# Kernel optimization log

Measured on AMD Instinct MI355X. Metric: run time of the kernel, lower is better.

Reference implementation:

```python
import jax, jax.numpy as jnp
import numpy as np

B, N, T = 1, 1024, 2048   # batch, graph nodes, timesteps
E, K = 16384, 32          # edges, causal kernel taps


def setup_inputs() -> dict:
    key = jax.random.key(0)
    k1, k2, k3, k4 = jax.random.split(key, 4)
    x = jax.random.normal(k1, (B, N, T), dtype=jnp.float32)
    # per-edge causal impulse-response kernels (aggregator(g) output)
    kernel = jax.random.normal(k2, (E, K), dtype=jnp.float32) * 0.1
    src = jax.random.randint(k3, (E,), 0, N)
    dst = jax.random.randint(k4, (E,), 0, N)
    return {"x": x, "kernel": kernel, "src": src, "dst": dst}


def reference(x, kernel, src, dst):
    # Block-sparse causal conv over the edge list:
    #   y_e[b, t] = sum_k kernel[e, k] * x[b, src_e, t - k]   (causal)
    #   out[b, n, t] = x[b, n, t] + sum_{e: dst_e = n} y_e[b, t]
    # (residual applied because g.include_index_diag is False)
    xs = x[:, src, :]                      # [B, E, T] gather upstream signals
    rhs = kernel[:, None, ::-1]            # [E, 1, K] flipped -> true causal conv
    y = jax.lax.conv_general_dilated(
        xs, rhs,
        window_strides=(1,),
        padding=[(K - 1, 0)],              # left-pad: strictly causal
        dimension_numbers=("NCW", "OIW", "NCW"),
        feature_group_count=E,             # one independent kernel per edge
    )                                      # [B, E, T]
    agg = jax.ops.segment_sum(jnp.swapaxes(y, 0, 1), dst, num_segments=N)  # [N, B, T]
    return x + jnp.swapaxes(agg, 0, 1)     # [B, N, T]
```

## Files before the change

kernel.cpp:

```cpp
#include <hip/hip_runtime.h>
#include <hip/hip_bf16.h>

#define TT  2048
#define KK  32
#define NN  1024
#define EE  16384
#define CAP 64
#define RS  2080

typedef short short8  __attribute__((ext_vector_type(8)));
typedef short short4v __attribute__((ext_vector_type(4)));
typedef float f32x4   __attribute__((ext_vector_type(4)));

__device__ short g_xbf[NN * RS];
__device__ short g_kbf[EE * KK];

__device__ __forceinline__ short f2bf(float f) {
    __hip_bfloat16 h = __float2bfloat16(f);
    return __builtin_bit_cast(short, h);
}

__global__ __launch_bounds__(256) void cvt_kernel(const float* __restrict__ x,
                                                  const float* __restrict__ kern,
                                                  int* __restrict__ cnt) {
    const int bid = blockIdx.x, tid = threadIdx.x;
    if (bid < NN) {
        const float4* xr = (const float4*)(x + (size_t)bid * TT);
        const float4 u = xr[2 * tid], v = xr[2 * tid + 1];
        short8 h;
        h[0]=f2bf(u.x); h[1]=f2bf(u.y); h[2]=f2bf(u.z); h[3]=f2bf(u.w);
        h[4]=f2bf(v.x); h[5]=f2bf(v.y); h[6]=f2bf(v.z); h[7]=f2bf(v.w);
        *(short8*)&g_xbf[(size_t)bid * RS + 32 + 8 * tid] = h;
        if (tid < 4) {
            short8 z; z[0]=0;z[1]=0;z[2]=0;z[3]=0;z[4]=0;z[5]=0;z[6]=0;z[7]=0;
            *(short8*)&g_xbf[(size_t)bid * RS + 8 * tid] = z;
        }
    } else if (bid == NN) {
        ((int4*)cnt)[tid] = make_int4(0, 0, 0, 0);
    } else {
        const int i = (bid - NN - 1) * 256 + tid;
        const float4* k4 = (const float4*)kern;
        const float4 u = k4[2 * i], v = k4[2 * i + 1];
        short8 h;
        h[0]=f2bf(u.x); h[1]=f2bf(u.y); h[2]=f2bf(u.z); h[3]=f2bf(u.w);
        h[4]=f2bf(v.x); h[5]=f2bf(v.y); h[6]=f2bf(v.z); h[7]=f2bf(v.w);
        ((short8*)g_kbf)[i] = h;
    }
}

__global__ __launch_bounds__(256) void csr_kernel(const int* __restrict__ src,
                                                  const int* __restrict__ dst,
                                                  int* __restrict__ cnt,
                                                  unsigned* __restrict__ slots) {
    const int e = blockIdx.x * 256 + threadIdx.x;
    const int d = dst[e];
    const int p = atomicAdd(&cnt[d], 1);
    if (p < CAP) slots[(size_t)d * CAP + p] = ((unsigned)src[e] << 14) | (unsigned)e;
}

__global__ __launch_bounds__(256, 4) void lti_kernel(
    const float*    __restrict__ x,
    const int*      __restrict__ cnt,
    const unsigned* __restrict__ slots,
    float*          __restrict__ out)
{
    const int n   = blockIdx.x;
    const int tid = threadIdx.x;
    const int w   = tid >> 6;
    const int ln  = tid & 63;
    const int c   = ln & 15, g = ln >> 4;
    const int t0  = 512 * w;
    const int D   = 16 * c + 8 * g;

    __shared__ __align__(16) short kt_all[4][8][72];
    __shared__ unsigned bl[CAP];

    short (*kt)[72] = kt_all[w];

    short8 z8; z8[0]=0;z8[1]=0;z8[2]=0;z8[3]=0;z8[4]=0;z8[5]=0;z8[6]=0;z8[7]=0;

    {
        short8* kz = (short8*)&kt[0][0];
        kz[ln] = z8;
        if (ln < 8) kz[64 + ln] = z8;
    }
    if (tid < CAP) bl[tid] = slots[(size_t)n * CAP + tid];
    int L = cnt[n]; if (L > CAP) L = CAP;
    __syncthreads();

    f32x4 acc0 = {0,0,0,0}, acc1 = {0,0,0,0};
    short8  xa0A, xb0A, xa1A, xb1A, xa0B, xb0B, xa1B, xb1B;
    short4v trA, trB;

    const int a_ = c & 7;
    const int s1 = ((a_ + 1) & 7) + 15 - c + 8 * g;

    #define LOADV(S, P)                                                                \
    {                                                                                  \
        const unsigned sv = bl[P];                                                     \
        const int e0 = __builtin_amdgcn_readfirstlane((int)(sv & 16383u));             \
        const int s0 = __builtin_amdgcn_readfirstlane((int)(sv >> 14));                \
        const short* rb = g_xbf + (size_t)s0 * RS + t0 + D;                            \
        xa0##S = *(const short8*)(rb);                                                 \
        xb0##S = *(const short8*)(rb + 16);                                            \
        xa1##S = *(const short8*)(rb + 256);                                           \
        xb1##S = *(const short8*)(rb + 272);                                           \
        tr##S  = *(const short4v*)(g_kbf + ((size_t)e0 << 5) + 4 * (ln & 7));          \
    }

    #define COMMIT(S)                                                                  \
    {                                                                                  \
        const int a2 = ln >> 3, pad = (a2 + 1) & 7, mb = 4 * (ln & 7);                 \
        kt[a2][pad + 47 - mb] = tr##S[0];                                              \
        kt[a2][pad + 46 - mb] = tr##S[1];                                              \
        kt[a2][pad + 45 - mb] = tr##S[2];                                              \
        kt[a2][pad + 44 - mb] = tr##S[3];                                              \
    }

    #define COMPUTE(S)                                                                 \
    {                                                                                  \
        const short8 b1 = *(const short8*)&kt[a_][s1];                                 \
        short8 b2 = *(const short8*)&kt[a_][s1 + 16];                                  \
        if (g < 2) b2 = z8;                              \
        acc0 = __builtin_amdgcn_mfma_f32_16x16x32_bf16(xa0##S, b1, acc0, 0, 0, 0);     \
        acc0 = __builtin_amdgcn_mfma_f32_16x16x32_bf16(xb0##S, b2, acc0, 0, 0, 0);     \
        acc1 = __builtin_amdgcn_mfma_f32_16x16x32_bf16(xa1##S, b1, acc1, 0, 0, 0);     \
        acc1 = __builtin_amdgcn_mfma_f32_16x16x32_bf16(xb1##S, b2, acc1, 0, 0, 0);     \
    }

    if (L > 0) {
        LOADV(A, 0);
        if (L > 1) LOADV(B, 1);
        for (int i = 0; i < L; i += 2) {
            COMMIT(A);
            COMPUTE(A);
            if (i + 2 < L) LOADV(A, i + 2);
            if (i + 1 < L) { COMMIT(B); COMPUTE(B); }
            if (i + 3 < L) LOADV(B, i + 3);
        }
    }

    const float* xr  = x   + (size_t)n * TT + t0;
    float*       orw = out + (size_t)n * TT + t0;
    #pragma unroll
    for (int qd = 0; qd < 4; ++qd) {
        const int ta = 64 * g + 16 * qd + c;
        orw[ta]       = xr[ta]       + acc0[qd];
        orw[256 + ta] = xr[256 + ta] + acc1[qd];
    }
    #undef LOADV
    #undef COMMIT
    #undef COMPUTE
}

extern "C" void kernel_launch(void* const* d_in, const int* in_sizes, int n_in,
                              void* d_out, int out_size, void* d_ws, size_t ws_size,
                              hipStream_t stream) {
    const float* x    = (const float*)d_in[0];
    const float* kern = (const float*)d_in[1];
    const int*   src  = (const int*)d_in[2];
    const int*   dst  = (const int*)d_in[3];
    float*       out  = (float*)d_out;

    int*      cnt   = (int*)d_ws;
    unsigned* slots = (unsigned*)((char*)d_ws + 4096);

    cvt_kernel<<<dim3(NN + 1 + EE * KK / 8 / 256), dim3(256), 0, stream>>>(x, kern, cnt);
    csr_kernel<<<dim3(EE / 256), dim3(256), 0, stream>>>(src, dst, cnt, slots);
    lti_kernel<<<dim3(NN), dim3(256), 0, stream>>>(x, cnt, slots, out);
}
```

Baseline: 38.30 us.

## Split edge list across two waves per time chunk with LDS reduction

Changes the LTI kernel from one block per node with four waves covering time chunks, to four blocks per node (one per time chunk), each with two waves that split the node's incoming edges by parity. Partial accumulators are reduced through shared memory before the residual add and store. This halves the serial edge-loop length per wave to shorten the critical path and adds more blocks for load balance, at the cost of an extra barrier, LDS reduction traffic, and duplicated slot/count loads per block.

```diff
diff --git a/kernel.cpp b/kernel.cpp
--- a/kernel.cpp
+++ b/kernel.cpp
@@ -58,24 +58,27 @@
     if (p < CAP) slots[(size_t)d * CAP + p] = ((unsigned)src[e] << 14) | (unsigned)e;
 }
 
-__global__ __launch_bounds__(256, 4) void lti_kernel(
+__global__ __launch_bounds__(128, 6) void lti_kernel(
     const float*    __restrict__ x,
     const int*      __restrict__ cnt,
     const unsigned* __restrict__ slots,
     float*          __restrict__ out)
 {
-    const int n   = blockIdx.x;
+    const int bid = blockIdx.x;
+    const int n   = bid >> 2;
+    const int w   = bid & 3;
     const int tid = threadIdx.x;
-    const int w   = tid >> 6;
+    const int pw  = tid >> 6;
     const int ln  = tid & 63;
     const int c   = ln & 15, g = ln >> 4;
     const int t0  = 512 * w;
     const int D   = 16 * c + 8 * g;
 
-    __shared__ __align__(16) short kt_all[4][8][72];
+    __shared__ __align__(16) short kt_all[2][8][72];
+    __shared__ __align__(16) float red[512];
     __shared__ unsigned bl[CAP];
 
-    short (*kt)[72] = kt_all[w];
+    short (*kt)[72] = kt_all[pw];
 
     short8 z8; z8[0]=0;z8[1]=0;z8[2]=0;z8[3]=0;z8[4]=0;z8[5]=0;z8[6]=0;z8[7]=0;
 
@@ -87,6 +90,9 @@
     if (tid < CAP) bl[tid] = slots[(size_t)n * CAP + tid];
     int L = cnt[n]; if (L > CAP) L = CAP;
     __syncthreads();
+
+    const int M = (L - pw + 1) >> 1;
+    #define IDX(I) (pw + 2 * (I))
 
     f32x4 acc0 = {0,0,0,0}, acc1 = {0,0,0,0};
     short8  xa0A, xb0A, xa1A, xb1A, xa0B, xb0B, xa1B, xb1B;
@@ -128,26 +134,38 @@
         acc1 = __builtin_amdgcn_mfma_f32_16x16x32_bf16(xb1##S, b2, acc1, 0, 0, 0);     \
     }
 
-    if (L > 0) {
-        LOADV(A, 0);
-        if (L > 1) LOADV(B, 1);
-        for (int i = 0; i < L; i += 2) {
+    if (M > 0) {
+        LOADV(A, IDX(0));
+        if (M > 1) LOADV(B, IDX(1));
+        for (int i = 0; i < M; i += 2) {
             COMMIT(A);
             COMPUTE(A);
-            if (i + 2 < L) LOADV(A, i + 2);
-            if (i + 1 < L) { COMMIT(B); COMPUTE(B); }
-            if (i + 3 < L) LOADV(B, i + 3);
+            if (i + 2 < M) LOADV(A, IDX(i + 2));
+            if (i + 1 < M) { COMMIT(B); COMPUTE(B); }
+            if (i + 3 < M) LOADV(B, IDX(i + 3));
         }
     }
 
-    const float* xr  = x   + (size_t)n * TT + t0;
-    float*       orw = out + (size_t)n * TT + t0;
-    #pragma unroll
-    for (int qd = 0; qd < 4; ++qd) {
-        const int ta = 64 * g + 16 * qd + c;
-        orw[ta]       = xr[ta]       + acc0[qd];
-        orw[256 + ta] = xr[256 + ta] + acc1[qd];
+    if (pw == 1) {
+        #pragma unroll
+        for (int qd = 0; qd < 4; ++qd) {
+            const int ta = 64 * g + 16 * qd + c;
+            red[ta]       = acc0[qd];
+            red[256 + ta] = acc1[qd];
+        }
     }
+    __syncthreads();
+    if (pw == 0) {
+        const float* xr  = x   + (size_t)n * TT + t0;
+        float*       orw = out + (size_t)n * TT + t0;
+        #pragma unroll
+        for (int qd = 0; qd < 4; ++qd) {
+            const int ta = 64 * g + 16 * qd + c;
+            orw[ta]       = xr[ta]       + acc0[qd] + red[ta];
+            orw[256 + ta] = xr[256 + ta] + acc1[qd] + red[256 + ta];
+        }
+    }
+    #undef IDX
     #undef LOADV
     #undef COMMIT
     #undef COMPUTE
@@ -167,5 +185,5 @@
 
     cvt_kernel<<<dim3(NN + 1 + EE * KK / 8 / 256), dim3(256), 0, stream>>>(x, kern, cnt);
     csr_kernel<<<dim3(EE / 256), dim3(256), 0, stream>>>(src, dst, cnt, slots);
-    lti_kernel<<<dim3(NN), dim3(256), 0, stream>>>(x, cnt, slots, out);
+    lti_kernel<<<dim3(NN * 4), dim3(128), 0, stream>>>(x, cnt, slots, out);
 }
```

Result: faster. 35.87 us (-6.4%).
